# Kernel optimization log

Measured on AMD Instinct MI355X. Metric: run time of the kernel, lower is better.

The kernel has to match this reference:

```python
import jax, jax.numpy as jnp
import numpy as np

B, CIN, COUT, G = 1, 64, 64, 1
NLAT, NLON = 256, 512
LMAX, MMAX = NLAT, NLON // 2 + 1  # torch-harmonics: lmax=nlat, mmax=nlon//2+1


def _legpoly(mmax, lmax, cost):
    """Fully (ortho) normalized associated Legendre \bar P_l^m(cos t), shape [mmax, lmax, nlat]."""
    nlat = cost.shape[0]
    p = np.zeros((mmax, lmax, nlat), dtype=np.float64)
    sint = np.sqrt(1.0 - cost * cost)
    pmm = np.full(nlat, np.sqrt(1.0 / (4.0 * np.pi)))  # \bar P_0^0
    for m in range(mmax):
        if m < lmax:
            p[m, m] = pmm
        if m + 1 < lmax:
            p[m, m + 1] = np.sqrt(2.0 * m + 3.0) * cost * pmm
        for l in range(m + 2, lmax):
            a = np.sqrt((4.0 * l * l - 1.0) / (l * l - m * m))
            b = np.sqrt(((l - 1.0) ** 2 - m * m) / (4.0 * (l - 1.0) ** 2 - 1.0))
            p[m, l] = a * (cost * p[m, l - 1] - b * p[m, l - 2])
        # diagonal step: \bar P_{m+1}^{m+1}
        pmm = -np.sqrt((2.0 * m + 3.0) / (2.0 * m + 2.0)) * sint * pmm
    return p


def setup_inputs():
    key = jax.random.key(0)
    k1, k2, k3 = jax.random.split(key, 3)
    # Gauss-Legendre nodes/weights (grid='legendre-gauss')
    cost, wq = np.polynomial.legendre.leggauss(NLAT)
    pct = _legpoly(MMAX, LMAX, cost)                      # [m, l, k] - ISHT matrix
    sht_w = pct * wq[None, None, :]                        # [m, l, k] - SHT matrix (Legendre * quadrature)
    x = jax.random.normal(k1, (B, CIN, NLAT, NLON), jnp.float32)
    # weight init: scale = sqrt(1/(Cin/g)), scale[0] *= sqrt(2); complex randn has var 1/2 per component
    scale = np.full(LMAX, np.sqrt(1.0 / (CIN // G)), np.float32)
    scale[0] *= np.sqrt(2.0)
    scale = scale * np.sqrt(0.5)
    weight_r = jax.random.normal(k2, (G, CIN // G, COUT // G, LMAX), jnp.float32) * scale
    weight_i = jax.random.normal(k3, (G, CIN // G, COUT // G, LMAX), jnp.float32) * scale
    return {"x": x, "weight_r": weight_r, "weight_i": weight_i,
            "pct": jnp.asarray(pct.astype(np.float32)),
            "sht_w": jnp.asarray(sht_w.astype(np.float32))}


def reference(x, weight_r, weight_i, pct, sht_w):
    residual = x  # scale_residual is False (same in/out shape and grid)
    x = x.astype(jnp.float32)
    # --- forward real SHT: rfft over lon, Legendre transform over lat ---
    xf = 2.0 * jnp.pi * jnp.fft.rfft(x, axis=-1, norm="forward")          # [B,C,k,m] complex64
    coeffs = jnp.einsum('bckm,mlk->bclm', xf, sht_w.astype(xf.dtype))      # [B,C,l,m]
    Bd, C, L, M = coeffs.shape
    # --- grouped per-l complex weight contraction (_contract_lwise) ---
    w = (weight_r + 1j * weight_i).astype(coeffs.dtype)                    # [g,i,o,l]
    xg = coeffs.reshape(Bd, G, C // G, L, M)
    out = jnp.einsum('bgilm,giol->bgolm', xg, w).reshape(Bd, COUT, L, M)
    # --- inverse real SHT ---
    xk = jnp.einsum('bolm,mlk->bokm', out, pct.astype(out.dtype))          # [B,Cout,k,m]
    y = jnp.fft.irfft(xk, n=NLON, axis=-1, norm="forward")                 # [B,Cout,nlat,nlon]
    return (y.astype(residual.dtype), residual)
```

## Files before the change

### kernel.cpp

```cpp
#include <hip/hip_runtime.h>

typedef _Float16 f16;
typedef _Float16 h8 __attribute__((ext_vector_type(8)));
typedef float f4 __attribute__((ext_vector_type(4)));

#define NLON 512
#define NLAT 256
#define NC   64
#define NM   256
#define NL   256
#define RTOT (NC*NLAT)

#define BO_FTR 0
#define BO_FTI (BO_FTR + 262144)
#define BO_GR  (BO_FTI + 262144)
#define BO_GI  (BO_GR  + 262144)
#define BO_WTR (BO_GI  + 262144)
#define BO_WTI (BO_WTR + 2097152)
#define BO_XFRE (BO_WTI + 2097152)
#define BO_XFIM (BO_XFRE + 8388608)
#define BO_PRE  (BO_XFIM + 8388608)
#define BO_PIM  (BO_PRE + 8388608)
#define BO_QRE  (BO_PIM + 8388608)
#define BO_QIM  (BO_QRE + 8388608)

__device__ inline f4 mfma16(h8 a, h8 b, f4 c) {
  return __builtin_amdgcn_mfma_f32_16x16x32_f16(a, b, c, 0, 0, 0);
}

__global__ void k_tables_h(f16* __restrict__ Ftr, f16* __restrict__ Fti,
                           f16* __restrict__ Gr, f16* __restrict__ Gi) {
  int idx = blockIdx.x * blockDim.x + threadIdx.x;
  if (idx >= NLON * NM) return;
  const float step = 3.14159265358979323846f / 256.0f;
  {
    int m = idx >> 9, n = idx & 511;
    int t = (n * m) & (NLON - 1);
    float th = t * step;
    const float sc = 6.2831853071795864769f / 512.0f;
    Ftr[idx] = (f16)(sc * cosf(th));
    Fti[idx] = (f16)(-sc * sinf(th));
  }
  {
    int n = idx >> 8, m = idx & 255;
    int t = (n * m) & (NLON - 1);
    float th = t * step;
    float s = (m == 0) ? 1.0f : 2.0f;
    Gr[idx] = (f16)(s * cosf(th));
    Gi[idx] = (f16)(-s * sinf(th));
  }
}

__global__ void k_permw_h(const float* __restrict__ w, f16* __restrict__ wT) {
  __shared__ float tile[32][33];
  int o = blockIdx.z;
  int i0 = blockIdx.y * 32;
  int l0 = blockIdx.x * 32;
  int xx = threadIdx.x, yy = threadIdx.y;
  for (int j = 0; j < 32; j += 8)
    tile[yy + j][xx] = w[(size_t)(i0 + yy + j) * (NC * NL) + (size_t)o * NL + l0 + xx];
  __syncthreads();
  for (int j = 0; j < 32; j += 8)
    wT[(size_t)(l0 + yy + j) * (NC * NC) + (size_t)o * NC + i0 + xx] = (f16)tile[xx][yy + j];
}

__global__ __launch_bounds__(256) void k_s1(
    const float* __restrict__ x, const f16* __restrict__ Ftr,
    const f16* __restrict__ Fti, f16* __restrict__ XFre, f16* __restrict__ XFim) {
  __shared__ f16 Ar[64][40], Ai[64][40], Bx[64][40];
  int t = threadIdx.x;
  int m0 = blockIdx.x * 64, r0 = blockIdx.y * 64;
  int lane = t & 63, w = t >> 6;
  int wm = (w >> 1) * 32, wn = (w & 1) * 32;
  int fr = lane & 15, kg = (lane >> 4) * 8;
  int srow = t >> 2, skc = (t & 3) * 8;
  f4 aR[2][2] = {}, aI[2][2] = {};
  for (int n0 = 0; n0 < NLON; n0 += 32) {
    *(h8*)&Ar[srow][skc] = *(const h8*)(Ftr + (size_t)(m0 + srow) * NLON + n0 + skc);
    *(h8*)&Ai[srow][skc] = *(const h8*)(Fti + (size_t)(m0 + srow) * NLON + n0 + skc);
    const float* px = x + (size_t)(r0 + srow) * NLON + n0 + skc;
    float4 v0 = *(const float4*)px;
    float4 v1 = *(const float4*)(px + 4);
    h8 hx = {(f16)v0.x, (f16)v0.y, (f16)v0.z, (f16)v0.w,
             (f16)v1.x, (f16)v1.y, (f16)v1.z, (f16)v1.w};
    *(h8*)&Bx[srow][skc] = hx;
    __syncthreads();
    h8 a0 = *(h8*)&Ar[wm + fr][kg],      a1 = *(h8*)&Ar[wm + 16 + fr][kg];
    h8 c0 = *(h8*)&Ai[wm + fr][kg],      c1 = *(h8*)&Ai[wm + 16 + fr][kg];
    h8 b0 = *(h8*)&Bx[wn + fr][kg],      b1 = *(h8*)&Bx[wn + 16 + fr][kg];
    aR[0][0] = mfma16(a0, b0, aR[0][0]); aR[0][1] = mfma16(a0, b1, aR[0][1]);
    aR[1][0] = mfma16(a1, b0, aR[1][0]); aR[1][1] = mfma16(a1, b1, aR[1][1]);
    aI[0][0] = mfma16(c0, b0, aI[0][0]); aI[0][1] = mfma16(c0, b1, aI[0][1]);
    aI[1][0] = mfma16(c1, b0, aI[1][0]); aI[1][1] = mfma16(c1, b1, aI[1][1]);
    __syncthreads();
  }
  int drow = (lane >> 4) * 4, dcol = lane & 15;
#pragma unroll
  for (int i = 0; i < 2; ++i)
#pragma unroll
    for (int j = 0; j < 2; ++j)
#pragma unroll
      for (int b = 0; b < 4; ++b) {
        size_t o = (size_t)(m0 + wm + i * 16 + drow + b) * RTOT + r0 + wn + j * 16 + dcol;
        XFre[o] = (f16)aR[i][j][b];
        XFim[o] = (f16)aI[i][j][b];
      }
}

__global__ __launch_bounds__(256) void k_s2(
    const f16* __restrict__ XFre, const f16* __restrict__ XFim,
    const float* __restrict__ shtw, f16* __restrict__ Pre, f16* __restrict__ Pim) {
  int m = blockIdx.y;
  int l0 = blockIdx.x * 64;
  int t = threadIdx.x;
  if (l0 + 64 <= m) {
    h8 z = {};
#pragma unroll
    for (int rep = 0; rep < 2; ++rep) {
      int f = rep * 256 + t;
      int ll = f >> 3, c8 = (f & 7) * 8;
      size_t o = (size_t)(l0 + ll) * RTOT + (size_t)m * 64 + c8;
      *(h8*)(Pre + o) = z;
      *(h8*)(Pim + o) = z;
    }
    return;
  }
  __shared__ f16 SH[9216];
  f16* Ar = SH;
  f16* Ai = SH + 2560;
  f16* Bs = SH + 5120;
  int lane = t & 63, w = t >> 6;
  int wm = (w >> 1) * 32, wn = (w & 1) * 32;
  int fr = lane & 15, kg = (lane >> 4) * 8;
  int srow = t >> 2, skc = (t & 3) * 8;
  const f16* Abr = XFre + (size_t)m * RTOT;
  const f16* Abi = XFim + (size_t)m * RTOT;
  const float* Bb = shtw + (size_t)m * (NL * NLAT);
  f4 aR[2][2] = {}, aI[2][2] = {};
  for (int k0 = 0; k0 < NLAT; k0 += 32) {
    *(h8*)&Ar[srow * 40 + skc] = *(const h8*)(Abr + (size_t)srow * NLAT + k0 + skc);
    *(h8*)&Ai[srow * 40 + skc] = *(const h8*)(Abi + (size_t)srow * NLAT + k0 + skc);
    const float* pb = Bb + (size_t)(l0 + srow) * NLAT + k0 + skc;
    float4 v0 = *(const float4*)pb;
    float4 v1 = *(const float4*)(pb + 4);
    h8 hb = {(f16)v0.x, (f16)v0.y, (f16)v0.z, (f16)v0.w,
             (f16)v1.x, (f16)v1.y, (f16)v1.z, (f16)v1.w};
    *(h8*)&Bs[srow * 40 + skc] = hb;
    __syncthreads();
    h8 a0 = *(h8*)&Ar[(wm + fr) * 40 + kg],      a1 = *(h8*)&Ar[(wm + 16 + fr) * 40 + kg];
    h8 c0 = *(h8*)&Ai[(wm + fr) * 40 + kg],      c1 = *(h8*)&Ai[(wm + 16 + fr) * 40 + kg];
    h8 b0 = *(h8*)&Bs[(wn + fr) * 40 + kg],      b1 = *(h8*)&Bs[(wn + 16 + fr) * 40 + kg];
    aR[0][0] = mfma16(a0, b0, aR[0][0]); aR[0][1] = mfma16(a0, b1, aR[0][1]);
    aR[1][0] = mfma16(a1, b0, aR[1][0]); aR[1][1] = mfma16(a1, b1, aR[1][1]);
    aI[0][0] = mfma16(c0, b0, aI[0][0]); aI[0][1] = mfma16(c0, b1, aI[0][1]);
    aI[1][0] = mfma16(c1, b0, aI[1][0]); aI[1][1] = mfma16(c1, b1, aI[1][1]);
    __syncthreads();
  }
  f16* Tr = SH;
  f16* Ti = SH + 4608;
  int drow = (lane >> 4) * 4, dcol = lane & 15;
#pragma unroll
  for (int i = 0; i < 2; ++i)
#pragma unroll
    for (int j = 0; j < 2; ++j)
#pragma unroll
      for (int b = 0; b < 4; ++b) {
        int c = wm + i * 16 + drow + b;
        int l = wn + j * 16 + dcol;
        Tr[l * 72 + c] = (f16)aR[i][j][b];
        Ti[l * 72 + c] = (f16)aI[i][j][b];
      }
  __syncthreads();
#pragma unroll
  for (int rep = 0; rep < 4; ++rep) {
    int f = rep * 256 + t;
    int buf = f >> 9, idx = f & 511;
    int ll = idx >> 3, c8 = (idx & 7) * 8;
    const f16* T = buf ? Ti : Tr;
    h8 v = *(const h8*)&T[ll * 72 + c8];
    f16* Pd = buf ? Pim : Pre;
    *(h8*)(Pd + (size_t)(l0 + ll) * RTOT + (size_t)m * 64 + c8) = v;
  }
}

__global__ __launch_bounds__(256) void k_s3(
    const f16* __restrict__ Pre, const f16* __restrict__ Pim,
    const f16* __restrict__ wTr, const f16* __restrict__ wTi,
    f16* __restrict__ Qre, f16* __restrict__ Qim) {
  int l = blockIdx.y;
  int m0 = blockIdx.x * 64;
  int t = threadIdx.x;
  size_t obase = (size_t)l * RTOT + (size_t)m0 * 64;
  if (m0 > l) {
    h8 z = {};
#pragma unroll
    for (int rep = 0; rep < 2; ++rep) {
      int f = rep * 256 + t;
      ((h8*)(Qre + obase))[f] = z;
      ((h8*)(Qim + obase))[f] = z;
    }
    return;
  }
  __shared__ f16 SH[18432];
  f16* Ar = SH;
  f16* Ai = SH + 4608;
  f16* Br = SH + 9216;
  f16* Bi = SH + 13824;
  const f16* Pbr = Pre + (size_t)l * RTOT + (size_t)m0 * 64;
  const f16* Pbi = Pim + (size_t)l * RTOT + (size_t)m0 * 64;
  const f16* Wbr = wTr + (size_t)l * 4096;
  const f16* Wbi = wTi + (size_t)l * 4096;
#pragma unroll
  for (int rep = 0; rep < 2; ++rep) {
    int f = rep * 256 + t;
    int row = f >> 3, c8 = (f & 7) * 8;
    *(h8*)&Ar[row * 72 + c8] = *(const h8*)(Pbr + (size_t)row * 64 + c8);
    *(h8*)&Ai[row * 72 + c8] = *(const h8*)(Pbi + (size_t)row * 64 + c8);
    *(h8*)&Br[row * 72 + c8] = *(const h8*)(Wbr + (size_t)f * 8);
    *(h8*)&Bi[row * 72 + c8] = *(const h8*)(Wbi + (size_t)f * 8);
  }
  __syncthreads();
  int lane = t & 63, w = t >> 6;
  int wm = (w >> 1) * 32, wn = (w & 1) * 32;
  int fr = lane & 15, kg = (lane >> 4) * 8;
  f4 RR[2][2] = {}, II[2][2] = {}, RI[2][2] = {}, IR[2][2] = {};
#pragma unroll
  for (int ks = 0; ks < 64; ks += 32) {
    h8 a0 = *(h8*)&Ar[(wm + fr) * 72 + ks + kg];
    h8 a1 = *(h8*)&Ar[(wm + 16 + fr) * 72 + ks + kg];
    h8 c0 = *(h8*)&Ai[(wm + fr) * 72 + ks + kg];
    h8 c1 = *(h8*)&Ai[(wm + 16 + fr) * 72 + ks + kg];
    h8 b0 = *(h8*)&Br[(wn + fr) * 72 + ks + kg];
    h8 b1 = *(h8*)&Br[(wn + 16 + fr) * 72 + ks + kg];
    h8 d0 = *(h8*)&Bi[(wn + fr) * 72 + ks + kg];
    h8 d1 = *(h8*)&Bi[(wn + 16 + fr) * 72 + ks + kg];
    RR[0][0] = mfma16(a0, b0, RR[0][0]); RR[0][1] = mfma16(a0, b1, RR[0][1]);
    RR[1][0] = mfma16(a1, b0, RR[1][0]); RR[1][1] = mfma16(a1, b1, RR[1][1]);
    II[0][0] = mfma16(c0, d0, II[0][0]); II[0][1] = mfma16(c0, d1, II[0][1]);
    II[1][0] = mfma16(c1, d0, II[1][0]); II[1][1] = mfma16(c1, d1, II[1][1]);
    RI[0][0] = mfma16(a0, d0, RI[0][0]); RI[0][1] = mfma16(a0, d1, RI[0][1]);
    RI[1][0] = mfma16(a1, d0, RI[1][0]); RI[1][1] = mfma16(a1, d1, RI[1][1]);
    IR[0][0] = mfma16(c0, b0, IR[0][0]); IR[0][1] = mfma16(c0, b1, IR[0][1]);
    IR[1][0] = mfma16(c1, b0, IR[1][0]); IR[1][1] = mfma16(c1, b1, IR[1][1]);
  }
  __syncthreads();
  f16* Tr = SH;
  f16* Ti = SH + 4608;
  int drow = (lane >> 4) * 4, dcol = lane & 15;
#pragma unroll
  for (int i = 0; i < 2; ++i)
#pragma unroll
    for (int j = 0; j < 2; ++j)
#pragma unroll
      for (int b = 0; b < 4; ++b) {
        int mm = wm + i * 16 + drow + b;
        int oo = wn + j * 16 + dcol;
        Tr[mm * 72 + oo] = (f16)(RR[i][j][b] - II[i][j][b]);
        Ti[mm * 72 + oo] = (f16)(RI[i][j][b] + IR[i][j][b]);
      }
  __syncthreads();
#pragma unroll
  for (int rep = 0; rep < 4; ++rep) {
    int f = rep * 256 + t;
    int buf = f >> 9, idx = f & 511;
    int mm = idx >> 3, o8 = (idx & 7) * 8;
    const f16* T = buf ? Ti : Tr;
    h8 v = *(const h8*)&T[mm * 72 + o8];
    f16* Qd = buf ? Qim : Qre;
    *(h8*)(Qd + obase + (size_t)mm * 64 + o8) = v;
  }
}

__global__ __launch_bounds__(256) void k_s4(
    const f16* __restrict__ Qre, const f16* __restrict__ Qim,
    const float* __restrict__ pct, f16* __restrict__ XKre, f16* __restrict__ XKim) {
  __shared__ f16 As[32 * 66], Ais[32 * 66], Bs[32 * 66];
  int m = blockIdx.y;
  int k0b = blockIdx.x * 64;
  int t = threadIdx.x;
  int lane = t & 63, w = t >> 6;
  int wm = (w >> 1) * 32, wn = (w & 1) * 32;
  int fr = lane & 15, kg = (lane >> 4) * 8;
  int lr = t >> 3, c8 = (t & 7) * 8;
  const float* Bb = pct + (size_t)m * (NL * NLAT);
  f4 aR[2][2] = {}, aI[2][2] = {};
  int lstart = m & ~31;
  for (int l0 = lstart; l0 < NL; l0 += 32) {
    *(h8*)&As[lr * 66 + c8]  = *(const h8*)(Qre + (size_t)(l0 + lr) * RTOT + (size_t)m * 64 + c8);
    *(h8*)&Ais[lr * 66 + c8] = *(const h8*)(Qim + (size_t)(l0 + lr) * RTOT + (size_t)m * 64 + c8);
    const float* pb = Bb + (size_t)(l0 + lr) * NLAT + k0b + c8;
    float4 v0 = *(const float4*)pb;
    float4 v1 = *(const float4*)(pb + 4);
    h8 hb = {(f16)v0.x, (f16)v0.y, (f16)v0.z, (f16)v0.w,
             (f16)v1.x, (f16)v1.y, (f16)v1.z, (f16)v1.w};
    *(h8*)&Bs[lr * 66 + c8] = hb;
    __syncthreads();
    h8 a0, a1, c0, c1, b0, b1;
#pragma unroll
    for (int e = 0; e < 8; ++e) {
      int row = (kg + e) * 66;
      a0[e] = As[row + wm + fr];
      a1[e] = As[row + wm + 16 + fr];
      c0[e] = Ais[row + wm + fr];
      c1[e] = Ais[row + wm + 16 + fr];
      b0[e] = Bs[row + wn + fr];
      b1[e] = Bs[row + wn + 16 + fr];
    }
    aR[0][0] = mfma16(a0, b0, aR[0][0]); aR[0][1] = mfma16(a0, b1, aR[0][1]);
    aR[1][0] = mfma16(a1, b0, aR[1][0]); aR[1][1] = mfma16(a1, b1, aR[1][1]);
    aI[0][0] = mfma16(c0, b0, aI[0][0]); aI[0][1] = mfma16(c0, b1, aI[0][1]);
    aI[1][0] = mfma16(c1, b0, aI[1][0]); aI[1][1] = mfma16(c1, b1, aI[1][1]);
    __syncthreads();
  }
  int drow = (lane >> 4) * 4, dcol = lane & 15;
#pragma unroll
  for (int i = 0; i < 2; ++i)
#pragma unroll
    for (int j = 0; j < 2; ++j)
#pragma unroll
      for (int b = 0; b < 4; ++b) {
        size_t o = (size_t)m * RTOT + (size_t)(wm + i * 16 + drow + b) * NLAT + k0b + wn + j * 16 + dcol;
        XKre[o] = (f16)aR[i][j][b];
        XKim[o] = (f16)aI[i][j][b];
      }
}

__global__ __launch_bounds__(256) void k_s5(
    const f16* __restrict__ XKre, const f16* __restrict__ XKim,
    const f16* __restrict__ Gr, const f16* __restrict__ Gi,
    float* __restrict__ y) {
  __shared__ f16 Ar[32 * 66], Ai[32 * 66], Br[64 * 34], Bi[64 * 34];
  int t = threadIdx.x;
  int n0 = blockIdx.x * 64, r0 = blockIdx.y * 64;
  int lane = t & 63, w = t >> 6;
  int wm = (w >> 1) * 32, wn = (w & 1) * 32;
  int fr = lane & 15, kg = (lane >> 4) * 8;
  int mr = t >> 3, r8 = (t & 7) * 8;
  int srow = t >> 2, skc = (t & 3) * 8;
  f4 acc[2][2] = {};
  for (int m0 = 0; m0 < NM; m0 += 32) {
    *(h8*)&Ar[mr * 66 + r8] = *(const h8*)(XKre + (size_t)(m0 + mr) * RTOT + r0 + r8);
    *(h8*)&Ai[mr * 66 + r8] = *(const h8*)(XKim + (size_t)(m0 + mr) * RTOT + r0 + r8);
    *(h8*)&Br[srow * 34 + skc] = *(const h8*)(Gr + (size_t)(n0 + srow) * NM + m0 + skc);
    *(h8*)&Bi[srow * 34 + skc] = *(const h8*)(Gi + (size_t)(n0 + srow) * NM + m0 + skc);
    __syncthreads();
    h8 a0, a1, c0, c1;
#pragma unroll
    for (int e = 0; e < 8; ++e) {
      int row = (kg + e) * 66;
      a0[e] = Ar[row + wm + fr];
      a1[e] = Ar[row + wm + 16 + fr];
      c0[e] = Ai[row + wm + fr];
      c1[e] = Ai[row + wm + 16 + fr];
    }
    h8 b0 = *(h8*)&Br[(wn + fr) * 34 + kg], b1 = *(h8*)&Br[(wn + 16 + fr) * 34 + kg];
    h8 d0 = *(h8*)&Bi[(wn + fr) * 34 + kg], d1 = *(h8*)&Bi[(wn + 16 + fr) * 34 + kg];
    acc[0][0] = mfma16(a0, b0, acc[0][0]); acc[0][1] = mfma16(a0, b1, acc[0][1]);
    acc[1][0] = mfma16(a1, b0, acc[1][0]); acc[1][1] = mfma16(a1, b1, acc[1][1]);
    acc[0][0] = mfma16(c0, d0, acc[0][0]); acc[0][1] = mfma16(c0, d1, acc[0][1]);
    acc[1][0] = mfma16(c1, d0, acc[1][0]); acc[1][1] = mfma16(c1, d1, acc[1][1]);
    __syncthreads();
  }
  int drow = (lane >> 4) * 4, dcol = lane & 15;
#pragma unroll
  for (int i = 0; i < 2; ++i)
#pragma unroll
    for (int j = 0; j < 2; ++j)
#pragma unroll
      for (int b = 0; b < 4; ++b)
        y[(size_t)(r0 + wm + i * 16 + drow + b) * NLON + n0 + wn + j * 16 + dcol] = acc[i][j][b];
}

extern "C" void kernel_launch(void* const* d_in, const int* in_sizes, int n_in,
                              void* d_out, int out_size, void* d_ws, size_t ws_size,
                              hipStream_t stream) {
  const float* x    = (const float*)d_in[0];
  const float* wgr  = (const float*)d_in[1];
  const float* wgi  = (const float*)d_in[2];
  const float* pct  = (const float*)d_in[3];
  const float* shtw = (const float*)d_in[4];
  float* out = (float*)d_out;
  char* ws = (char*)d_ws;

  f16* Ftr = (f16*)(ws + BO_FTR);
  f16* Fti = (f16*)(ws + BO_FTI);
  f16* Gr  = (f16*)(ws + BO_GR);
  f16* Gi  = (f16*)(ws + BO_GI);
  f16* wTr = (f16*)(ws + BO_WTR);
  f16* wTi = (f16*)(ws + BO_WTI);
  f16* XFre = (f16*)(ws + BO_XFRE);
  f16* XFim = (f16*)(ws + BO_XFIM);
  f16* Pre  = (f16*)(ws + BO_PRE);
  f16* Pim  = (f16*)(ws + BO_PIM);
  f16* Qre  = (f16*)(ws + BO_QRE);
  f16* Qim  = (f16*)(ws + BO_QIM);

  hipLaunchKernelGGL(k_tables_h, dim3(512), dim3(256), 0, stream, Ftr, Fti, Gr, Gi);
  hipLaunchKernelGGL(k_permw_h, dim3(8, 2, 64), dim3(32, 8), 0, stream, wgr, wTr);
  hipLaunchKernelGGL(k_permw_h, dim3(8, 2, 64), dim3(32, 8), 0, stream, wgi, wTi);
  hipLaunchKernelGGL(k_s1, dim3(4, 256), dim3(256), 0, stream, x, Ftr, Fti, XFre, XFim);
  hipLaunchKernelGGL(k_s2, dim3(4, 256), dim3(256), 0, stream, XFre, XFim, shtw, Pre, Pim);
  hipLaunchKernelGGL(k_s3, dim3(4, 256), dim3(256), 0, stream, Pre, Pim, wTr, wTi, Qre, Qim);
  hipLaunchKernelGGL(k_s4, dim3(4, 256), dim3(256), 0, stream, Qre, Qim, pct, XFre, XFim);
  hipLaunchKernelGGL(k_s5, dim3(8, 256), dim3(256), 0, stream, XFre, XFim, Gr, Gi, out);
  hipMemcpyAsync(out + (size_t)NC * NLAT * NLON, x,
                 sizeof(float) * NC * NLAT * NLON, hipMemcpyDeviceToDevice, stream);
}
```

Baseline: 134.7 us.

## Enlarge GEMM tiles in s1/s4/s5, fuse residual copy and weight permutes

Doubles the per-block output tile in the forward DFT, inverse Legendre and inverse DFT GEMMs, so each wave computes twice as many MFMA tiles per shared-memory load of the reused operand and the grids shrink accordingly. The residual copy of x is folded into k_s1, which already reads x, replacing a separate device-to-device memcpy. The two weight-permute launches are merged into one. The larger tiles raise register and LDS use, and halve the block count, which may reduce occupancy.

```diff
diff --git a/kernel.cpp b/kernel.cpp
--- a/kernel.cpp
+++ b/kernel.cpp
@@ -51,9 +51,13 @@
   }
 }
 
-__global__ void k_permw_h(const float* __restrict__ w, f16* __restrict__ wT) {
+__global__ void k_permw2(const float* __restrict__ wr, const float* __restrict__ wi,
+                         f16* __restrict__ wTr, f16* __restrict__ wTi) {
   __shared__ float tile[32][33];
-  int o = blockIdx.z;
+  int z = blockIdx.z;
+  int o = z >> 1;
+  const float* w = (z & 1) ? wi : wr;
+  f16* wT = (z & 1) ? wTi : wTr;
   int i0 = blockIdx.y * 32;
   int l0 = blockIdx.x * 32;
   int xx = threadIdx.x, yy = threadIdx.y;
@@ -66,44 +70,59 @@
 
 __global__ __launch_bounds__(256) void k_s1(
     const float* __restrict__ x, const f16* __restrict__ Ftr,
-    const f16* __restrict__ Fti, f16* __restrict__ XFre, f16* __restrict__ XFim) {
-  __shared__ f16 Ar[64][40], Ai[64][40], Bx[64][40];
+    const f16* __restrict__ Fti, f16* __restrict__ XFre, f16* __restrict__ XFim,
+    float* __restrict__ res) {
+  __shared__ f16 Ar[128 * 40], Ai[128 * 40], Bx[64 * 40];
   int t = threadIdx.x;
-  int m0 = blockIdx.x * 64, r0 = blockIdx.y * 64;
+  int m0 = blockIdx.x * 128, r0 = blockIdx.y * 64;
   int lane = t & 63, w = t >> 6;
   int wm = (w >> 1) * 32, wn = (w & 1) * 32;
   int fr = lane & 15, kg = (lane >> 4) * 8;
   int srow = t >> 2, skc = (t & 3) * 8;
-  f4 aR[2][2] = {}, aI[2][2] = {};
+  f4 aR[4][2] = {}, aI[4][2] = {};
   for (int n0 = 0; n0 < NLON; n0 += 32) {
-    *(h8*)&Ar[srow][skc] = *(const h8*)(Ftr + (size_t)(m0 + srow) * NLON + n0 + skc);
-    *(h8*)&Ai[srow][skc] = *(const h8*)(Fti + (size_t)(m0 + srow) * NLON + n0 + skc);
+#pragma unroll
+    for (int rep = 0; rep < 2; ++rep) {
+      int f = rep * 256 + t;
+      int row = f >> 2, c8 = (f & 3) * 8;
+      *(h8*)&Ar[row * 40 + c8] = *(const h8*)(Ftr + (size_t)(m0 + row) * NLON + n0 + c8);
+      *(h8*)&Ai[row * 40 + c8] = *(const h8*)(Fti + (size_t)(m0 + row) * NLON + n0 + c8);
+    }
     const float* px = x + (size_t)(r0 + srow) * NLON + n0 + skc;
     float4 v0 = *(const float4*)px;
     float4 v1 = *(const float4*)(px + 4);
+    if (blockIdx.x == 0) {
+      float* pr = res + (size_t)(r0 + srow) * NLON + n0 + skc;
+      *(float4*)pr = v0;
+      *(float4*)(pr + 4) = v1;
+    }
     h8 hx = {(f16)v0.x, (f16)v0.y, (f16)v0.z, (f16)v0.w,
              (f16)v1.x, (f16)v1.y, (f16)v1.z, (f16)v1.w};
-    *(h8*)&Bx[srow][skc] = hx;
-    __syncthreads();
-    h8 a0 = *(h8*)&Ar[wm + fr][kg],      a1 = *(h8*)&Ar[wm + 16 + fr][kg];
-    h8 c0 = *(h8*)&Ai[wm + fr][kg],      c1 = *(h8*)&Ai[wm + 16 + fr][kg];
-    h8 b0 = *(h8*)&Bx[wn + fr][kg],      b1 = *(h8*)&Bx[wn + 16 + fr][kg];
-    aR[0][0] = mfma16(a0, b0, aR[0][0]); aR[0][1] = mfma16(a0, b1, aR[0][1]);
-    aR[1][0] = mfma16(a1, b0, aR[1][0]); aR[1][1] = mfma16(a1, b1, aR[1][1]);
-    aI[0][0] = mfma16(c0, b0, aI[0][0]); aI[0][1] = mfma16(c0, b1, aI[0][1]);
-    aI[1][0] = mfma16(c1, b0, aI[1][0]); aI[1][1] = mfma16(c1, b1, aI[1][1]);
+    *(h8*)&Bx[srow * 40 + skc] = hx;
+    __syncthreads();
+    h8 b0 = *(h8*)&Bx[(wn + fr) * 40 + kg];
+    h8 b1 = *(h8*)&Bx[(wn + 16 + fr) * 40 + kg];
+#pragma unroll
+    for (int im = 0; im < 4; ++im) {
+      int mrow = wm + (im >> 1) * 64 + (im & 1) * 16 + fr;
+      h8 a = *(h8*)&Ar[mrow * 40 + kg];
+      h8 c = *(h8*)&Ai[mrow * 40 + kg];
+      aR[im][0] = mfma16(a, b0, aR[im][0]); aR[im][1] = mfma16(a, b1, aR[im][1]);
+      aI[im][0] = mfma16(c, b0, aI[im][0]); aI[im][1] = mfma16(c, b1, aI[im][1]);
+    }
     __syncthreads();
   }
   int drow = (lane >> 4) * 4, dcol = lane & 15;
 #pragma unroll
-  for (int i = 0; i < 2; ++i)
+  for (int im = 0; im < 4; ++im)
 #pragma unroll
     for (int j = 0; j < 2; ++j)
 #pragma unroll
       for (int b = 0; b < 4; ++b) {
-        size_t o = (size_t)(m0 + wm + i * 16 + drow + b) * RTOT + r0 + wn + j * 16 + dcol;
-        XFre[o] = (f16)aR[i][j][b];
-        XFim[o] = (f16)aI[i][j][b];
+        int mg = m0 + wm + (im >> 1) * 64 + (im & 1) * 16 + drow + b;
+        size_t o = (size_t)mg * RTOT + r0 + wn + j * 16 + dcol;
+        XFre[o] = (f16)aR[im][j][b];
+        XFim[o] = (f16)aI[im][j][b];
       }
 }
 
@@ -274,28 +293,37 @@
 __global__ __launch_bounds__(256) void k_s4(
     const f16* __restrict__ Qre, const f16* __restrict__ Qim,
     const float* __restrict__ pct, f16* __restrict__ XKre, f16* __restrict__ XKim) {
-  __shared__ f16 As[32 * 66], Ais[32 * 66], Bs[32 * 66];
+  __shared__ f16 As[32 * 66], Ais[32 * 66], Bs0[32 * 66], Bs1[32 * 66];
   int m = blockIdx.y;
-  int k0b = blockIdx.x * 64;
+  int k0b = blockIdx.x * 128;
   int t = threadIdx.x;
   int lane = t & 63, w = t >> 6;
   int wm = (w >> 1) * 32, wn = (w & 1) * 32;
   int fr = lane & 15, kg = (lane >> 4) * 8;
   int lr = t >> 3, c8 = (t & 7) * 8;
   const float* Bb = pct + (size_t)m * (NL * NLAT);
-  f4 aR[2][2] = {}, aI[2][2] = {};
+  f4 aR[2][4] = {}, aI[2][4] = {};
   int lstart = m & ~31;
   for (int l0 = lstart; l0 < NL; l0 += 32) {
     *(h8*)&As[lr * 66 + c8]  = *(const h8*)(Qre + (size_t)(l0 + lr) * RTOT + (size_t)m * 64 + c8);
     *(h8*)&Ais[lr * 66 + c8] = *(const h8*)(Qim + (size_t)(l0 + lr) * RTOT + (size_t)m * 64 + c8);
     const float* pb = Bb + (size_t)(l0 + lr) * NLAT + k0b + c8;
-    float4 v0 = *(const float4*)pb;
-    float4 v1 = *(const float4*)(pb + 4);
-    h8 hb = {(f16)v0.x, (f16)v0.y, (f16)v0.z, (f16)v0.w,
-             (f16)v1.x, (f16)v1.y, (f16)v1.z, (f16)v1.w};
-    *(h8*)&Bs[lr * 66 + c8] = hb;
-    __syncthreads();
-    h8 a0, a1, c0, c1, b0, b1;
+    {
+      float4 v0 = *(const float4*)pb;
+      float4 v1 = *(const float4*)(pb + 4);
+      h8 hb = {(f16)v0.x, (f16)v0.y, (f16)v0.z, (f16)v0.w,
+               (f16)v1.x, (f16)v1.y, (f16)v1.z, (f16)v1.w};
+      *(h8*)&Bs0[lr * 66 + c8] = hb;
+    }
+    {
+      float4 v0 = *(const float4*)(pb + 64);
+      float4 v1 = *(const float4*)(pb + 68);
+      h8 hb = {(f16)v0.x, (f16)v0.y, (f16)v0.z, (f16)v0.w,
+               (f16)v1.x, (f16)v1.y, (f16)v1.z, (f16)v1.w};
+      *(h8*)&Bs1[lr * 66 + c8] = hb;
+    }
+    __syncthreads();
+    h8 a0, a1, c0, c1, b0, b1, b2, b3;
 #pragma unroll
     for (int e = 0; e < 8; ++e) {
       int row = (kg + e) * 66;
@@ -303,23 +331,31 @@
       a1[e] = As[row + wm + 16 + fr];
       c0[e] = Ais[row + wm + fr];
       c1[e] = Ais[row + wm + 16 + fr];
-      b0[e] = Bs[row + wn + fr];
-      b1[e] = Bs[row + wn + 16 + fr];
+      b0[e] = Bs0[row + wn + fr];
+      b1[e] = Bs0[row + wn + 16 + fr];
+      b2[e] = Bs1[row + wn + fr];
+      b3[e] = Bs1[row + wn + 16 + fr];
     }
     aR[0][0] = mfma16(a0, b0, aR[0][0]); aR[0][1] = mfma16(a0, b1, aR[0][1]);
+    aR[0][2] = mfma16(a0, b2, aR[0][2]); aR[0][3] = mfma16(a0, b3, aR[0][3]);
     aR[1][0] = mfma16(a1, b0, aR[1][0]); aR[1][1] = mfma16(a1, b1, aR[1][1]);
+    aR[1][2] = mfma16(a1, b2, aR[1][2]); aR[1][3] = mfma16(a1, b3, aR[1][3]);
     aI[0][0] = mfma16(c0, b0, aI[0][0]); aI[0][1] = mfma16(c0, b1, aI[0][1]);
+    aI[0][2] = mfma16(c0, b2, aI[0][2]); aI[0][3] = mfma16(c0, b3, aI[0][3]);
     aI[1][0] = mfma16(c1, b0, aI[1][0]); aI[1][1] = mfma16(c1, b1, aI[1][1]);
+    aI[1][2] = mfma16(c1, b2, aI[1][2]); aI[1][3] = mfma16(c1, b3, aI[1][3]);
     __syncthreads();
   }
   int drow = (lane >> 4) * 4, dcol = lane & 15;
 #pragma unroll
   for (int i = 0; i < 2; ++i)
 #pragma unroll
-    for (int j = 0; j < 2; ++j)
+    for (int j = 0; j < 4; ++j)
 #pragma unroll
       for (int b = 0; b < 4; ++b) {
-        size_t o = (size_t)m * RTOT + (size_t)(wm + i * 16 + drow + b) * NLAT + k0b + wn + j * 16 + dcol;
+        int orow = wm + i * 16 + drow + b;
+        int kcol = k0b + (j >> 1) * 64 + (j & 1) * 16 + wn + dcol;
+        size_t o = (size_t)m * RTOT + (size_t)orow * NLAT + kcol;
         XKre[o] = (f16)aR[i][j][b];
         XKim[o] = (f16)aI[i][j][b];
       }
@@ -329,20 +365,24 @@
     const f16* __restrict__ XKre, const f16* __restrict__ XKim,
     const f16* __restrict__ Gr, const f16* __restrict__ Gi,
     float* __restrict__ y) {
-  __shared__ f16 Ar[32 * 66], Ai[32 * 66], Br[64 * 34], Bi[64 * 34];
+  __shared__ f16 Ar[32 * 66], Ai[32 * 66], Br[128 * 34], Bi[128 * 34];
   int t = threadIdx.x;
-  int n0 = blockIdx.x * 64, r0 = blockIdx.y * 64;
+  int n0 = blockIdx.x * 128, r0 = blockIdx.y * 64;
   int lane = t & 63, w = t >> 6;
   int wm = (w >> 1) * 32, wn = (w & 1) * 32;
   int fr = lane & 15, kg = (lane >> 4) * 8;
   int mr = t >> 3, r8 = (t & 7) * 8;
-  int srow = t >> 2, skc = (t & 3) * 8;
-  f4 acc[2][2] = {};
+  f4 acc[2][4] = {};
   for (int m0 = 0; m0 < NM; m0 += 32) {
     *(h8*)&Ar[mr * 66 + r8] = *(const h8*)(XKre + (size_t)(m0 + mr) * RTOT + r0 + r8);
     *(h8*)&Ai[mr * 66 + r8] = *(const h8*)(XKim + (size_t)(m0 + mr) * RTOT + r0 + r8);
-    *(h8*)&Br[srow * 34 + skc] = *(const h8*)(Gr + (size_t)(n0 + srow) * NM + m0 + skc);
-    *(h8*)&Bi[srow * 34 + skc] = *(const h8*)(Gi + (size_t)(n0 + srow) * NM + m0 + skc);
+#pragma unroll
+    for (int rep = 0; rep < 2; ++rep) {
+      int f = rep * 256 + t;
+      int row = f >> 2, cc = (f & 3) * 8;
+      *(h8*)&Br[row * 34 + cc] = *(const h8*)(Gr + (size_t)(n0 + row) * NM + m0 + cc);
+      *(h8*)&Bi[row * 34 + cc] = *(const h8*)(Gi + (size_t)(n0 + row) * NM + m0 + cc);
+    }
     __syncthreads();
     h8 a0, a1, c0, c1;
 #pragma unroll
@@ -353,22 +393,29 @@
       c0[e] = Ai[row + wm + fr];
       c1[e] = Ai[row + wm + 16 + fr];
     }
-    h8 b0 = *(h8*)&Br[(wn + fr) * 34 + kg], b1 = *(h8*)&Br[(wn + 16 + fr) * 34 + kg];
-    h8 d0 = *(h8*)&Bi[(wn + fr) * 34 + kg], d1 = *(h8*)&Bi[(wn + 16 + fr) * 34 + kg];
-    acc[0][0] = mfma16(a0, b0, acc[0][0]); acc[0][1] = mfma16(a0, b1, acc[0][1]);
-    acc[1][0] = mfma16(a1, b0, acc[1][0]); acc[1][1] = mfma16(a1, b1, acc[1][1]);
-    acc[0][0] = mfma16(c0, d0, acc[0][0]); acc[0][1] = mfma16(c0, d1, acc[0][1]);
-    acc[1][0] = mfma16(c1, d0, acc[1][0]); acc[1][1] = mfma16(c1, d1, acc[1][1]);
+#pragma unroll
+    for (int j = 0; j < 4; ++j) {
+      int nb = wn + (j & 1) * 16 + (j >> 1) * 64;
+      h8 b = *(h8*)&Br[(nb + fr) * 34 + kg];
+      h8 d = *(h8*)&Bi[(nb + fr) * 34 + kg];
+      acc[0][j] = mfma16(a0, b, acc[0][j]);
+      acc[1][j] = mfma16(a1, b, acc[1][j]);
+      acc[0][j] = mfma16(c0, d, acc[0][j]);
+      acc[1][j] = mfma16(c1, d, acc[1][j]);
+    }
     __syncthreads();
   }
   int drow = (lane >> 4) * 4, dcol = lane & 15;
 #pragma unroll
   for (int i = 0; i < 2; ++i)
 #pragma unroll
-    for (int j = 0; j < 2; ++j)
-#pragma unroll
-      for (int b = 0; b < 4; ++b)
-        y[(size_t)(r0 + wm + i * 16 + drow + b) * NLON + n0 + wn + j * 16 + dcol] = acc[i][j][b];
+    for (int j = 0; j < 4; ++j)
+#pragma unroll
+      for (int b = 0; b < 4; ++b) {
+        int rg = r0 + wm + i * 16 + drow + b;
+        int ng = n0 + wn + (j & 1) * 16 + (j >> 1) * 64 + dcol;
+        y[(size_t)rg * NLON + ng] = acc[i][j][b];
+      }
 }
 
 extern "C" void kernel_launch(void* const* d_in, const int* in_sizes, int n_in,
@@ -395,14 +442,13 @@
   f16* Qre  = (f16*)(ws + BO_QRE);
   f16* Qim  = (f16*)(ws + BO_QIM);
 
+  float* res = out + (size_t)NC * NLAT * NLON;
+
   hipLaunchKernelGGL(k_tables_h, dim3(512), dim3(256), 0, stream, Ftr, Fti, Gr, Gi);
-  hipLaunchKernelGGL(k_permw_h, dim3(8, 2, 64), dim3(32, 8), 0, stream, wgr, wTr);
-  hipLaunchKernelGGL(k_permw_h, dim3(8, 2, 64), dim3(32, 8), 0, stream, wgi, wTi);
-  hipLaunchKernelGGL(k_s1, dim3(4, 256), dim3(256), 0, stream, x, Ftr, Fti, XFre, XFim);
+  hipLaunchKernelGGL(k_permw2, dim3(8, 2, 128), dim3(32, 8), 0, stream, wgr, wgi, wTr, wTi);
+  hipLaunchKernelGGL(k_s1, dim3(2, 256), dim3(256), 0, stream, x, Ftr, Fti, XFre, XFim, res);
   hipLaunchKernelGGL(k_s2, dim3(4, 256), dim3(256), 0, stream, XFre, XFim, shtw, Pre, Pim);
   hipLaunchKernelGGL(k_s3, dim3(4, 256), dim3(256), 0, stream, Pre, Pim, wTr, wTi, Qre, Qim);
-  hipLaunchKernelGGL(k_s4, dim3(4, 256), dim3(256), 0, stream, Qre, Qim, pct, XFre, XFim);
-  hipLaunchKernelGGL(k_s5, dim3(8, 256), dim3(256), 0, stream, XFre, XFim, Gr, Gi, out);
-  hipMemcpyAsync(out + (size_t)NC * NLAT * NLON, x,
-                 sizeof(float) * NC * NLAT * NLON, hipMemcpyDeviceToDevice, stream);
-}
+  hipLaunchKernelGGL(k_s4, dim3(2, 256), dim3(256), 0, stream, Qre, Qim, pct, XFre, XFim);
+  hipLaunchKernelGGL(k_s5, dim3(4, 256), dim3(256), 0, stream, XFre, XFim, Gr, Gi, out);
+}
```

Result: faster. 117.0 us (-13.2%).
